# Optimization experiments

Hardware: AMD Instinct MI355X
Metric: run time of the kernel (lower is better)

## Reference

```python
import jax, jax.numpy as jnp
import numpy as np

B, N, FIN, H, D = 2, 512, 128, 4, 64
NEG_SLOPE = 0.2


def setup_inputs() -> dict:
    key = jax.random.key(0)
    ks = jax.random.split(key, 5)
    x = jax.random.normal(ks[0], (B, N, FIN), dtype=jnp.float32)
    # xavier-ish scaled params
    W_proj = jax.random.normal(ks[1], (H, FIN, D), dtype=jnp.float32) * (1.0 / np.sqrt(FIN + D))
    b_proj = jnp.zeros((H, D), dtype=jnp.float32)
    W_cat_weight = jax.random.normal(ks[2], (H, D, 2 * D), dtype=jnp.float32) * (1.0 / np.sqrt(3 * D))
    W_cat_bias = jnp.zeros((H, D), dtype=jnp.float32)
    a = jax.random.normal(ks[3], (H, D), dtype=jnp.float32) * (1.0 / np.sqrt(D))
    bias_param = jnp.zeros((H * D,), dtype=jnp.float32)
    return {"x": x, "W_proj": W_proj, "b_proj": b_proj,
            "W_cat_weight": W_cat_weight, "W_cat_bias": W_cat_bias,
            "a": a, "bias_param": bias_param}


def reference(x, W_proj, b_proj, W_cat_weight, W_cat_bias, a, bias_param):
    # h[b,h,n,d] = W^h x_n + b^h
    h = jnp.einsum('bni,hid->bhnd', x, W_proj) + b_proj[None, :, None, :]
    d = h.shape[-1]
    # W_cat [h_i || h_j] == W1 h_i + W2 h_j  (avoids O(N^2*2D) concat tensor)
    W1 = W_cat_weight[:, :, :d]   # (H, D, D) acts on source node i
    W2 = W_cat_weight[:, :, d:]   # (H, D, D) acts on target node j
    zi = jnp.einsum('bhnd,hed->bhne', h, W1)  # (B,H,N,D)
    zj = jnp.einsum('bhnd,hed->bhne', h, W2)  # (B,H,N,D)
    # z[b,h,i,j,e] = zi[b,h,i,e] + zj[b,h,j,e] + bias, then LeakyReLU
    z = zi[:, :, :, None, :] + zj[:, :, None, :, :] + W_cat_bias[None, :, None, None, :]
    z = jnp.where(z >= 0, z, NEG_SLOPE * z)
    # e[b,h,i,j] = a_h . z
    e = jnp.einsum('bhije,he->bhij', z, a)
    attn = jax.nn.softmax(e, axis=-1)          # softmax over neighbors j
    out = jnp.einsum('bhij,bhjd->bhid', attn, h)  # (B,H,N,D)
    b_, h_, n_, d_ = out.shape
    out = out.transpose(0, 2, 1, 3).reshape(b_, n_, h_ * d_)  # concat heads
    out = out + bias_param
    return out
```

## Files before the change

kernel.cpp:

```cpp
#include <hip/hip_runtime.h>
#include <hip/hip_bf16.h>

#define NN 512
#define FIN 128
#define HH 4
#define DD 64
#define SW 68


__global__ __launch_bounds__(256) void proj_kernel(
    const float* __restrict__ x, const float* __restrict__ Wp,
    const float* __restrict__ bp, const float* __restrict__ Wc,
    const float* __restrict__ Wcb, const float* __restrict__ a,
    float* __restrict__ h_ws, float* __restrict__ azi_ws, float* __restrict__ azjT,
    float* __restrict__ adi_ws, float* __restrict__ adj_ws)
{
    int blk = blockIdx.x;
    int bh = blk >> 6;
    int n0 = (blk & 63) << 3;
    int b = bh >> 2, hh = bh & 3;

    __shared__ float xs[8 * FIN];
    __shared__ float hs[8][DD];
    __shared__ float Wcs[DD][2 * DD + 1];
    __shared__ float tzj[8][DD + 1];
    __shared__ int   slot2e[SW];
    __shared__ float slot2pa[SW];

    int t = threadIdx.x;

    ((float4*)xs)[t] = ((const float4*)(x + ((size_t)b * NN + n0) * FIN))[t];
    {
        const float4* wg = (const float4*)(Wc + (size_t)hh * DD * 2 * DD);
        #pragma unroll
        for (int k = 0; k < 8; ++k) {
            int idx = t + 256 * k;
            int r = idx >> 5, c4 = (idx & 31) * 4;
            float4 v = wg[idx];
            Wcs[r][c4] = v.x; Wcs[r][c4 + 1] = v.y;
            Wcs[r][c4 + 2] = v.z; Wcs[r][c4 + 3] = v.w;
        }
    }
    __syncthreads();

    int e = t & 63, w = t >> 6;
    const float* Wph = Wp + (size_t)hh * FIN * DD;
    float bpv = bp[hh * DD + e];
    float acc0 = bpv, acc1 = bpv;
    #pragma unroll 8
    for (int i = 0; i < FIN; ++i) {
        float wv = Wph[i * DD + e];
        acc0 = fmaf(xs[w * FIN + i], wv, acc0);
        acc1 = fmaf(xs[(w + 4) * FIN + i], wv, acc1);
    }
    hs[w][e] = acc0; hs[w + 4][e] = acc1;
    float* hg = h_ws + ((size_t)bh * NN + n0) * DD;
    hg[w * DD + e] = acc0; hg[(w + 4) * DD + e] = acc1;
    __syncthreads();

    float zb = Wcb[hh * DD + e];
    float zi0 = zb, zi1 = zb, zj0 = 0.f, zj1 = 0.f;
    #pragma unroll 8
    for (int d2 = 0; d2 < DD; ++d2) {
        float w1 = Wcs[e][d2];
        float w2 = Wcs[e][DD + d2];
        float h0 = hs[w][d2], h1 = hs[w + 4][d2];
        zi0 = fmaf(h0, w1, zi0); zi1 = fmaf(h1, w1, zi1);
        zj0 = fmaf(h0, w2, zj0); zj1 = fmaf(h1, w2, zj1);
    }
    tzj[w][e] = zj0; tzj[w + 4][e] = zj1;

    float av = a[hh * DD + e];
    float p0 = av * zi0, p1 = av * zi1, q0 = av * zj0, q1 = av * zj1;
    #pragma unroll
    for (int off = 32; off; off >>= 1) {
        p0 += __shfl_xor(p0, off); p1 += __shfl_xor(p1, off);
        q0 += __shfl_xor(q0, off); q1 += __shfl_xor(q1, off);
    }
    if (e == 0) {
        adi_ws[bh * NN + n0 + w]     = 0.6f * p0;
        adi_ws[bh * NN + n0 + w + 4] = 0.6f * p1;
        adj_ws[bh * NN + n0 + w]     = 0.6f * q0;
        adj_ws[bh * NN + n0 + w + 4] = 0.6f * q1;
    }

    unsigned long long mask = __ballot(av >= 0.f);
    int np = __popcll(mask);
    int GP = (np + 3) >> 2;
    int below = __popcll(mask & ((1ull << e) - 1ull));
    int slot = (av >= 0.f) ? below : (4 * GP + (e - below));
    float pav = __builtin_fabsf(av);

    float* azib = azi_ws + ((size_t)bh * NN + n0) * SW;
    azib[w * SW + slot]       = pav * zi0;
    azib[(w + 4) * SW + slot] = pav * zi1;
    if (w == 0) { slot2e[slot] = e; slot2pa[slot] = pav; }
    int p1c = 4 * GP - np;
    if (e < 4) {
        int psl = (e < p1c) ? (np + e) : (4 * GP + 64 - np + (e - p1c));
        azib[w * SW + psl] = 0.f; azib[(w + 4) * SW + psl] = 0.f;
        if (w == 0) { slot2e[psl] = 0; slot2pa[psl] = 0.f; }
    }
    __syncthreads();

    for (int idx = t; idx < SW * 8; idx += 256) {
        int slot = idx >> 3, r = idx & 7;
        float v = slot2pa[slot] * tzj[r][slot2e[slot]];
        azjT[((size_t)bh * SW + slot) * NN + n0 + r] = v;
    }
}

__global__ __launch_bounds__(256) void attn_kernel(
    const float* __restrict__ h_ws, const float* __restrict__ azi_ws,
    const float* __restrict__ azjT, const float* __restrict__ adi_ws,
    const float* __restrict__ adj_ws, const float* __restrict__ a,
    float* __restrict__ pacc, float* __restrict__ pm, float* __restrict__ ps)
{
    int blk = blockIdx.x;
    int js = blk & 7, it = (blk >> 3) & 63, bh = blk >> 9;
    int j0 = js << 6, i0 = it << 3, hh = bh & 3;

    __shared__ float azis[8 * SW];
    __shared__ float pbuf[8][64];
    __shared__ float htile[64 * 64];

    int t = threadIdx.x, lane = t & 63;
    int w = t >> 6;

    if (t < 136)
        ((float4*)azis)[t] = ((const float4*)(azi_ws + ((size_t)bh * NN + i0) * SW))[t];
    {
        const float4* hsrc = (const float4*)(h_ws + ((size_t)bh * NN + j0) * DD);
        float4* hdst = (float4*)htile;
        #pragma unroll
        for (int k = 0; k < 4; ++k) hdst[t + 256 * k] = hsrc[t + 256 * k];
    }

    float azjr[SW];
    {
        const float* ajT = azjT + (size_t)bh * SW * NN + j0 + lane;
        #pragma unroll
        for (int k = 0; k < SW; ++k) azjr[k] = ajT[(size_t)k * NN];
    }
    float adjv = adj_ws[bh * NN + j0 + lane];

    float av_e = a[hh * DD + lane];
    unsigned long long mask = __ballot(av_e >= 0.f);
    int GP = (__popcll(mask) + 3) >> 2;
    float sgn[17];
    #pragma unroll
    for (int k = 0; k < 17; ++k) sgn[k] = (k < GP) ? 0.4f : -0.4f;

    float adiA = adi_ws[bh * NN + i0 + 2 * w];
    float adiB = adi_ws[bh * NN + i0 + 2 * w + 1];

    __syncthreads();

    #pragma unroll
    for (int ii = 0; ii < 2; ++ii) {
        int i = 2 * w + ii;
        const float4* arow = (const float4*)(azis + i * SW);
        float acc0 = 0.f, acc1 = 0.f;
        #pragma unroll
        for (int k = 0; k < 17; ++k) {
            float4 zi4 = arow[k];
            float s = sgn[k];
            acc0 = fmaf(s, __builtin_fabsf(zi4.x + azjr[4 * k + 0]), acc0);
            acc1 = fmaf(s, __builtin_fabsf(zi4.y + azjr[4 * k + 1]), acc1);
            acc0 = fmaf(s, __builtin_fabsf(zi4.z + azjr[4 * k + 2]), acc0);
            acc1 = fmaf(s, __builtin_fabsf(zi4.w + azjr[4 * k + 3]), acc1);
        }
        float ev = ((ii == 0) ? adiA : adiB) + adjv + acc0 + acc1;
        float m = ev;
        #pragma unroll
        for (int off = 32; off; off >>= 1) m = fmaxf(m, __shfl_xor(m, off));
        float p = __expf(ev - m);
        float ssum = p;
        #pragma unroll
        for (int off = 32; off; off >>= 1) ssum += __shfl_xor(ssum, off);
        pbuf[i][lane] = p;
        if (lane == 0) {
            pm[(js * 8 + bh) * NN + i0 + i] = m;
            ps[(js * 8 + bh) * NN + i0 + i] = ssum;
        }
    }

    float accA = 0.f, accB = 0.f;
    const float4* pA = (const float4*)pbuf[2 * w];
    const float4* pB = (const float4*)pbuf[2 * w + 1];
    #pragma unroll
    for (int k = 0; k < 16; ++k) {
        float4 a4 = pA[k], b4 = pB[k];
        float h0 = htile[(4 * k + 0) * 64 + lane];
        float h1 = htile[(4 * k + 1) * 64 + lane];
        float h2 = htile[(4 * k + 2) * 64 + lane];
        float h3 = htile[(4 * k + 3) * 64 + lane];
        accA = fmaf(a4.x, h0, accA); accB = fmaf(b4.x, h0, accB);
        accA = fmaf(a4.y, h1, accA); accB = fmaf(b4.y, h1, accB);
        accA = fmaf(a4.z, h2, accA); accB = fmaf(b4.z, h2, accB);
        accA = fmaf(a4.w, h3, accA); accB = fmaf(b4.w, h3, accB);
    }
    size_t ob = ((size_t)(js * 8 + bh) * NN + i0 + 2 * w) * DD + lane;
    pacc[ob] = accA;
    pacc[ob + DD] = accB;
}

__global__ __launch_bounds__(256) void combine_kernel(
    const float* __restrict__ pacc, const float* __restrict__ pm,
    const float* __restrict__ ps, const float* __restrict__ bias_param,
    float* __restrict__ out)
{
    int tid = blockIdx.x * 256 + threadIdx.x;
    int d = tid & 63;
    int row = tid >> 6;
    int bh = row >> 9, n = row & 511;
    int b = bh >> 2, hh = bh & 3;
    float mv[8];
    float m = -1e30f;
    #pragma unroll
    for (int p = 0; p < 8; ++p) { mv[p] = pm[p * 4096 + row]; m = fmaxf(m, mv[p]); }
    float denom = 0.f, acc = 0.f;
    #pragma unroll
    for (int p = 0; p < 8; ++p) {
        float wgt = __expf(mv[p] - m);
        denom = fmaf(ps[p * 4096 + row], wgt, denom);
        acc = fmaf(pacc[(size_t)p * 262144 + (size_t)row * 64 + d], wgt, acc);
    }
    out[((size_t)b * NN + n) * (HH * DD) + hh * DD + d] =
        acc / denom + bias_param[hh * DD + d];
}

extern "C" void kernel_launch(void* const* d_in, const int* in_sizes, int n_in,
                              void* d_out, int out_size, void* d_ws, size_t ws_size,
                              hipStream_t stream) {
    const float* x    = (const float*)d_in[0];
    const float* Wp   = (const float*)d_in[1];
    const float* bp   = (const float*)d_in[2];
    const float* Wc   = (const float*)d_in[3];
    const float* Wcb  = (const float*)d_in[4];
    const float* a    = (const float*)d_in[5];
    const float* bpar = (const float*)d_in[6];
    float* out = (float*)d_out;

    float* ws     = (float*)d_ws;
    float* h_ws   = ws;
    float* azi_ws = ws + 262144;
    float* azjT   = ws + 540672;
    float* adi_ws = ws + 819200;
    float* adj_ws = ws + 823296;
    float* pacc   = ws + 827392;
    float* pm     = ws + 2924544;
    float* ps     = ws + 2957312;

    proj_kernel<<<dim3(512), dim3(256), 0, stream>>>(
        x, Wp, bp, Wc, Wcb, a, h_ws, azi_ws, azjT, adi_ws, adj_ws);
    attn_kernel<<<dim3(4096), dim3(256), 0, stream>>>(
        h_ws, azi_ws, azjT, adi_ws, adj_ws, a, pacc, pm, ps);
    combine_kernel<<<dim3(1024), dim3(256), 0, stream>>>(
        pacc, pm, ps, bpar, out);
}
```

Before: 44.67 us.

## Fuse split-j attention and combine into single online-softmax kernel

Replaces the split-neighbor attention kernel plus separate combine kernel with one kernel per (batch-head, 8-row tile) that iterates over all 8 neighbor tiles using an online softmax with running max and sum. This removes the partial accumulator/max/sum workspace writes and reads and one kernel launch. In exchange the grid drops from 4096 to 512 blocks, and each block serially loads tiles, so latency hiding and occupancy are reduced.

```diff
diff --git a/kernel.cpp b/kernel.cpp
--- a/kernel.cpp
+++ b/kernel.cpp
@@ -104,21 +104,22 @@
     __syncthreads();
 
     for (int idx = t; idx < SW * 8; idx += 256) {
-        int slot = idx >> 3, r = idx & 7;
-        float v = slot2pa[slot] * tzj[r][slot2e[slot]];
-        azjT[((size_t)bh * SW + slot) * NN + n0 + r] = v;
+        int sl = idx >> 3, r = idx & 7;
+        azjT[((size_t)bh * SW + sl) * NN + n0 + r] =
+            slot2pa[sl] * tzj[r][slot2e[sl]];
     }
 }
 
-__global__ __launch_bounds__(256) void attn_kernel(
+__global__ __launch_bounds__(256) void attn_full(
     const float* __restrict__ h_ws, const float* __restrict__ azi_ws,
     const float* __restrict__ azjT, const float* __restrict__ adi_ws,
     const float* __restrict__ adj_ws, const float* __restrict__ a,
-    float* __restrict__ pacc, float* __restrict__ pm, float* __restrict__ ps)
+    const float* __restrict__ bias_param, float* __restrict__ out)
 {
     int blk = blockIdx.x;
-    int js = blk & 7, it = (blk >> 3) & 63, bh = blk >> 9;
-    int j0 = js << 6, i0 = it << 3, hh = bh & 3;
+    int bh = blk >> 6, it = blk & 63;
+    int i0 = it << 3;
+    int b = bh >> 2, hh = bh & 3;
 
     __shared__ float azis[8 * SW];
     __shared__ float pbuf[8][64];
@@ -128,21 +129,8 @@
     int w = t >> 6;
 
     if (t < 136)
-        ((float4*)azis)[t] = ((const float4*)(azi_ws + ((size_t)bh * NN + i0) * SW))[t];
-    {
-        const float4* hsrc = (const float4*)(h_ws + ((size_t)bh * NN + j0) * DD);
-        float4* hdst = (float4*)htile;
-        #pragma unroll
-        for (int k = 0; k < 4; ++k) hdst[t + 256 * k] = hsrc[t + 256 * k];
-    }
-
-    float azjr[SW];
-    {
-        const float* ajT = azjT + (size_t)bh * SW * NN + j0 + lane;
-        #pragma unroll
-        for (int k = 0; k < SW; ++k) azjr[k] = ajT[(size_t)k * NN];
-    }
-    float adjv = adj_ws[bh * NN + j0 + lane];
+        ((float4*)azis)[t] =
+            ((const float4*)(azi_ws + ((size_t)bh * NN + i0) * SW))[t];
 
     float av_e = a[hh * DD + lane];
     unsigned long long mask = __ballot(av_e >= 0.f);
@@ -154,80 +142,80 @@
     float adiA = adi_ws[bh * NN + i0 + 2 * w];
     float adiB = adi_ws[bh * NN + i0 + 2 * w + 1];
 
-    __syncthreads();
-
-    #pragma unroll
-    for (int ii = 0; ii < 2; ++ii) {
-        int i = 2 * w + ii;
-        const float4* arow = (const float4*)(azis + i * SW);
-        float acc0 = 0.f, acc1 = 0.f;
+    float mrun0 = -1e30f, mrun1 = -1e30f;
+    float srun0 = 0.f, srun1 = 0.f;
+    float accA = 0.f, accB = 0.f;
+
+    for (int jt = 0; jt < 8; ++jt) {
+        __syncthreads();
+        {
+            const float4* hsrc =
+                (const float4*)(h_ws + ((size_t)bh * NN + jt * 64) * DD);
+            float4* hdst = (float4*)htile;
+            #pragma unroll
+            for (int k = 0; k < 4; ++k) hdst[t + 256 * k] = hsrc[t + 256 * k];
+        }
+        float azjr[SW];
+        {
+            const float* ajT = azjT + (size_t)bh * SW * NN + jt * 64 + lane;
+            #pragma unroll
+            for (int k = 0; k < SW; ++k) azjr[k] = ajT[(size_t)k * NN];
+        }
+        float adjv = adj_ws[bh * NN + jt * 64 + lane];
+        __syncthreads();
+
+        float sc0, sc1;
         #pragma unroll
-        for (int k = 0; k < 17; ++k) {
-            float4 zi4 = arow[k];
-            float s = sgn[k];
-            acc0 = fmaf(s, __builtin_fabsf(zi4.x + azjr[4 * k + 0]), acc0);
-            acc1 = fmaf(s, __builtin_fabsf(zi4.y + azjr[4 * k + 1]), acc1);
-            acc0 = fmaf(s, __builtin_fabsf(zi4.z + azjr[4 * k + 2]), acc0);
-            acc1 = fmaf(s, __builtin_fabsf(zi4.w + azjr[4 * k + 3]), acc1);
-        }
-        float ev = ((ii == 0) ? adiA : adiB) + adjv + acc0 + acc1;
-        float m = ev;
+        for (int ii = 0; ii < 2; ++ii) {
+            int i = 2 * w + ii;
+            const float4* arow = (const float4*)(azis + i * SW);
+            float c0 = 0.f, c1 = 0.f;
+            #pragma unroll
+            for (int k = 0; k < 17; ++k) {
+                float4 zi4 = arow[k];
+                float s = sgn[k];
+                c0 = fmaf(s, __builtin_fabsf(zi4.x + azjr[4 * k + 0]), c0);
+                c1 = fmaf(s, __builtin_fabsf(zi4.y + azjr[4 * k + 1]), c1);
+                c0 = fmaf(s, __builtin_fabsf(zi4.z + azjr[4 * k + 2]), c0);
+                c1 = fmaf(s, __builtin_fabsf(zi4.w + azjr[4 * k + 3]), c1);
+            }
+            float ev = ((ii == 0) ? adiA : adiB) + adjv + c0 + c1;
+            float mt = ev;
+            #pragma unroll
+            for (int off = 32; off; off >>= 1) mt = fmaxf(mt, __shfl_xor(mt, off));
+            float m_old = (ii == 0) ? mrun0 : mrun1;
+            float m_new = fmaxf(m_old, mt);
+            float sc = __expf(m_old - m_new);
+            float p = __expf(ev - m_new);
+            float psum = p;
+            #pragma unroll
+            for (int off = 32; off; off >>= 1) psum += __shfl_xor(psum, off);
+            if (ii == 0) { srun0 = srun0 * sc + psum; mrun0 = m_new; sc0 = sc; }
+            else         { srun1 = srun1 * sc + psum; mrun1 = m_new; sc1 = sc; }
+            pbuf[i][lane] = p;
+        }
+
+        accA *= sc0; accB *= sc1;
+        const float4* pA = (const float4*)pbuf[2 * w];
+        const float4* pB = (const float4*)pbuf[2 * w + 1];
         #pragma unroll
-        for (int off = 32; off; off >>= 1) m = fmaxf(m, __shfl_xor(m, off));
-        float p = __expf(ev - m);
-        float ssum = p;
-        #pragma unroll
-        for (int off = 32; off; off >>= 1) ssum += __shfl_xor(ssum, off);
-        pbuf[i][lane] = p;
-        if (lane == 0) {
-            pm[(js * 8 + bh) * NN + i0 + i] = m;
-            ps[(js * 8 + bh) * NN + i0 + i] = ssum;
-        }
-    }
-
-    float accA = 0.f, accB = 0.f;
-    const float4* pA = (const float4*)pbuf[2 * w];
-    const float4* pB = (const float4*)pbuf[2 * w + 1];
-    #pragma unroll
-    for (int k = 0; k < 16; ++k) {
-        float4 a4 = pA[k], b4 = pB[k];
-        float h0 = htile[(4 * k + 0) * 64 + lane];
-        float h1 = htile[(4 * k + 1) * 64 + lane];
-        float h2 = htile[(4 * k + 2) * 64 + lane];
-        float h3 = htile[(4 * k + 3) * 64 + lane];
-        accA = fmaf(a4.x, h0, accA); accB = fmaf(b4.x, h0, accB);
-        accA = fmaf(a4.y, h1, accA); accB = fmaf(b4.y, h1, accB);
-        accA = fmaf(a4.z, h2, accA); accB = fmaf(b4.z, h2, accB);
-        accA = fmaf(a4.w, h3, accA); accB = fmaf(b4.w, h3, accB);
-    }
-    size_t ob = ((size_t)(js * 8 + bh) * NN + i0 + 2 * w) * DD + lane;
-    pacc[ob] = accA;
-    pacc[ob + DD] = accB;
-}
-
-__global__ __launch_bounds__(256) void combine_kernel(
-    const float* __restrict__ pacc, const float* __restrict__ pm,
-    const float* __restrict__ ps, const float* __restrict__ bias_param,
-    float* __restrict__ out)
-{
-    int tid = blockIdx.x * 256 + threadIdx.x;
-    int d = tid & 63;
-    int row = tid >> 6;
-    int bh = row >> 9, n = row & 511;
-    int b = bh >> 2, hh = bh & 3;
-    float mv[8];
-    float m = -1e30f;
-    #pragma unroll
-    for (int p = 0; p < 8; ++p) { mv[p] = pm[p * 4096 + row]; m = fmaxf(m, mv[p]); }
-    float denom = 0.f, acc = 0.f;
-    #pragma unroll
-    for (int p = 0; p < 8; ++p) {
-        float wgt = __expf(mv[p] - m);
-        denom = fmaf(ps[p * 4096 + row], wgt, denom);
-        acc = fmaf(pacc[(size_t)p * 262144 + (size_t)row * 64 + d], wgt, acc);
-    }
-    out[((size_t)b * NN + n) * (HH * DD) + hh * DD + d] =
-        acc / denom + bias_param[hh * DD + d];
+        for (int k = 0; k < 16; ++k) {
+            float4 a4 = pA[k], b4 = pB[k];
+            float h0 = htile[(4 * k + 0) * 64 + lane];
+            float h1 = htile[(4 * k + 1) * 64 + lane];
+            float h2 = htile[(4 * k + 2) * 64 + lane];
+            float h3 = htile[(4 * k + 3) * 64 + lane];
+            accA = fmaf(a4.x, h0, accA); accB = fmaf(b4.x, h0, accB);
+            accA = fmaf(a4.y, h1, accA); accB = fmaf(b4.y, h1, accB);
+            accA = fmaf(a4.z, h2, accA); accB = fmaf(b4.z, h2, accB);
+            accA = fmaf(a4.w, h3, accA); accB = fmaf(b4.w, h3, accB);
+        }
+    }
+
+    float bpv = bias_param[hh * DD + lane];
+    int iA = i0 + 2 * w, iB = iA + 1;
+    out[((size_t)b * NN + iA) * (HH * DD) + hh * DD + lane] = accA / srun0 + bpv;
+    out[((size_t)b * NN + iB) * (HH * DD) + hh * DD + lane] = accB / srun1 + bpv;
 }
 
 extern "C" void kernel_launch(void* const* d_in, const int* in_sizes, int n_in,
@@ -248,14 +236,9 @@
     float* azjT   = ws + 540672;
     float* adi_ws = ws + 819200;
     float* adj_ws = ws + 823296;
-    float* pacc   = ws + 827392;
-    float* pm     = ws + 2924544;
-    float* ps     = ws + 2957312;
 
     proj_kernel<<<dim3(512), dim3(256), 0, stream>>>(
         x, Wp, bp, Wc, Wcb, a, h_ws, azi_ws, azjT, adi_ws, adj_ws);
-    attn_kernel<<<dim3(4096), dim3(256), 0, stream>>>(
-        h_ws, azi_ws, azjT, adi_ws, adj_ws, a, pacc, pm, ps);
-    combine_kernel<<<dim3(1024), dim3(256), 0, stream>>>(
-        pacc, pm, ps, bpar, out);
+    attn_full<<<dim3(512), dim3(256), 0, stream>>>(
+        h_ws, azi_ws, azjT, adi_ws, adj_ws, a, bpar, out);
 }
```

After: 57.14 us. 1.28x slower.

## Tile attention over 16 query rows, block-pack azj as float4, swizzle grid

Applied to the files above, without the earlier changes.

The attention kernel now handles 16 query rows per workgroup instead of 8, with each wave doing 4 rows. This halves the grid and reuses the per-lane azj registers and the h tile over twice as many rows. The projection kernel writes azj in a blocked float4 layout so each lane loads 17 coalesced float4 values instead of 68 strided scalars. The block index is swizzled so neighbouring workgroups share a j-slice, and launch bounds ask for 4 workgroups per CU. In exchange, register pressure and the per-row serial work per wave both go up.

```diff
diff --git a/kernel.cpp b/kernel.cpp
--- a/kernel.cpp
+++ b/kernel.cpp
@@ -12,7 +12,7 @@
     const float* __restrict__ x, const float* __restrict__ Wp,
     const float* __restrict__ bp, const float* __restrict__ Wc,
     const float* __restrict__ Wcb, const float* __restrict__ a,
-    float* __restrict__ h_ws, float* __restrict__ azi_ws, float* __restrict__ azjT,
+    float* __restrict__ h_ws, float* __restrict__ azi_ws, float* __restrict__ azjB,
     float* __restrict__ adi_ws, float* __restrict__ adj_ws)
 {
     int blk = blockIdx.x;
@@ -103,106 +103,125 @@
     }
     __syncthreads();
 
-    for (int idx = t; idx < SW * 8; idx += 256) {
-        int slot = idx >> 3, r = idx & 7;
-        float v = slot2pa[slot] * tzj[r][slot2e[slot]];
-        azjT[((size_t)bh * SW + slot) * NN + n0 + r] = v;
-    }
-}
-
-__global__ __launch_bounds__(256) void attn_kernel(
+    if (t < 8 * 17) {
+        int r = t / 17, g = t % 17;
+        float4 v;
+        v.x = slot2pa[4 * g + 0] * tzj[r][slot2e[4 * g + 0]];
+        v.y = slot2pa[4 * g + 1] * tzj[r][slot2e[4 * g + 1]];
+        v.z = slot2pa[4 * g + 2] * tzj[r][slot2e[4 * g + 2]];
+        v.w = slot2pa[4 * g + 3] * tzj[r][slot2e[4 * g + 3]];
+        int jt = n0 >> 6, jl = (n0 & 63) + r;
+        ((float4*)azjB)[((size_t)(bh * 8 + jt) * 17 + g) * 64 + jl] = v;
+    }
+}
+
+__global__ __launch_bounds__(256, 4) void attn3(
     const float* __restrict__ h_ws, const float* __restrict__ azi_ws,
-    const float* __restrict__ azjT, const float* __restrict__ adi_ws,
+    const float* __restrict__ azjB, const float* __restrict__ adi_ws,
     const float* __restrict__ adj_ws, const float* __restrict__ a,
     float* __restrict__ pacc, float* __restrict__ pm, float* __restrict__ ps)
 {
-    int blk = blockIdx.x;
-    int js = blk & 7, it = (blk >> 3) & 63, bh = blk >> 9;
-    int j0 = js << 6, i0 = it << 3, hh = bh & 3;
-
-    __shared__ float azis[8 * SW];
-    __shared__ float pbuf[8][64];
+    int wg = (blockIdx.x & 7) * 256 + (blockIdx.x >> 3);
+    int bh = wg >> 8, js = (wg >> 5) & 7, it = wg & 31;
+    int i0 = it << 4, j0 = js << 6;
+    int hh = bh & 3;
+
     __shared__ float htile[64 * 64];
+    __shared__ float azis[16 * SW];
+    __shared__ float pbuf[16][64];
 
     int t = threadIdx.x, lane = t & 63;
-    int w = t >> 6;
-
-    if (t < 136)
-        ((float4*)azis)[t] = ((const float4*)(azi_ws + ((size_t)bh * NN + i0) * SW))[t];
+    int w = __builtin_amdgcn_readfirstlane(t >> 6);
+
     {
         const float4* hsrc = (const float4*)(h_ws + ((size_t)bh * NN + j0) * DD);
         float4* hdst = (float4*)htile;
         #pragma unroll
         for (int k = 0; k < 4; ++k) hdst[t + 256 * k] = hsrc[t + 256 * k];
-    }
-
-    float azjr[SW];
+        const float4* zsrc = (const float4*)(azi_ws + ((size_t)bh * NN + i0) * SW);
+        float4* zdst = (float4*)azis;
+        zdst[t] = zsrc[t];
+        if (t < 16) zdst[256 + t] = zsrc[256 + t];
+    }
+
+    float4 azj[17];
     {
-        const float* ajT = azjT + (size_t)bh * SW * NN + j0 + lane;
-        #pragma unroll
-        for (int k = 0; k < SW; ++k) azjr[k] = ajT[(size_t)k * NN];
+        const float4* ajB = (const float4*)azjB
+                          + ((size_t)(bh * 8 + js) * 17) * 64 + lane;
+        #pragma unroll
+        for (int k = 0; k < 17; ++k) azj[k] = ajB[k * 64];
     }
     float adjv = adj_ws[bh * NN + j0 + lane];
 
     float av_e = a[hh * DD + lane];
     unsigned long long mask = __ballot(av_e >= 0.f);
     int GP = (__popcll(mask) + 3) >> 2;
-    float sgn[17];
-    #pragma unroll
-    for (int k = 0; k < 17; ++k) sgn[k] = (k < GP) ? 0.4f : -0.4f;
-
-    float adiA = adi_ws[bh * NN + i0 + 2 * w];
-    float adiB = adi_ws[bh * NN + i0 + 2 * w + 1];
-
-    __syncthreads();
-
-    #pragma unroll
-    for (int ii = 0; ii < 2; ++ii) {
-        int i = 2 * w + ii;
+
+    int r0 = i0 + 4 * w;
+    float adi0 = adi_ws[bh * NN + r0 + 0];
+    float adi1 = adi_ws[bh * NN + r0 + 1];
+    float adi2 = adi_ws[bh * NN + r0 + 2];
+    float adi3 = adi_ws[bh * NN + r0 + 3];
+
+    __syncthreads();
+
+    #pragma unroll
+    for (int ii = 0; ii < 4; ++ii) {
+        int i = 4 * w + ii;
         const float4* arow = (const float4*)(azis + i * SW);
-        float acc0 = 0.f, acc1 = 0.f;
+        float c0 = 0.f, c1 = 0.f, c2 = 0.f, c3 = 0.f;
         #pragma unroll
         for (int k = 0; k < 17; ++k) {
             float4 zi4 = arow[k];
-            float s = sgn[k];
-            acc0 = fmaf(s, __builtin_fabsf(zi4.x + azjr[4 * k + 0]), acc0);
-            acc1 = fmaf(s, __builtin_fabsf(zi4.y + azjr[4 * k + 1]), acc1);
-            acc0 = fmaf(s, __builtin_fabsf(zi4.z + azjr[4 * k + 2]), acc0);
-            acc1 = fmaf(s, __builtin_fabsf(zi4.w + azjr[4 * k + 3]), acc1);
+            float4 aj = azj[k];
+            float s = (k < GP) ? 0.4f : -0.4f;
+            c0 = fmaf(s, __builtin_fabsf(zi4.x + aj.x), c0);
+            c1 = fmaf(s, __builtin_fabsf(zi4.y + aj.y), c1);
+            c2 = fmaf(s, __builtin_fabsf(zi4.z + aj.z), c2);
+            c3 = fmaf(s, __builtin_fabsf(zi4.w + aj.w), c3);
         }
-        float ev = ((ii == 0) ? adiA : adiB) + adjv + acc0 + acc1;
+        float adiv = (ii == 0) ? adi0 : (ii == 1) ? adi1 : (ii == 2) ? adi2 : adi3;
+        float ev = adiv + adjv + ((c0 + c1) + (c2 + c3));
         float m = ev;
         #pragma unroll
         for (int off = 32; off; off >>= 1) m = fmaxf(m, __shfl_xor(m, off));
         float p = __expf(ev - m);
-        float ssum = p;
-        #pragma unroll
-        for (int off = 32; off; off >>= 1) ssum += __shfl_xor(ssum, off);
+        float s = p;
+        #pragma unroll
+        for (int off = 32; off; off >>= 1) s += __shfl_xor(s, off);
         pbuf[i][lane] = p;
         if (lane == 0) {
-            pm[(js * 8 + bh) * NN + i0 + i] = m;
-            ps[(js * 8 + bh) * NN + i0 + i] = ssum;
+            pm[js * 4096 + bh * NN + i0 + i] = m;
+            ps[js * 4096 + bh * NN + i0 + i] = s;
         }
     }
 
-    float accA = 0.f, accB = 0.f;
-    const float4* pA = (const float4*)pbuf[2 * w];
-    const float4* pB = (const float4*)pbuf[2 * w + 1];
+    float a0 = 0.f, a1 = 0.f, a2 = 0.f, a3 = 0.f;
     #pragma unroll
     for (int k = 0; k < 16; ++k) {
-        float4 a4 = pA[k], b4 = pB[k];
         float h0 = htile[(4 * k + 0) * 64 + lane];
         float h1 = htile[(4 * k + 1) * 64 + lane];
         float h2 = htile[(4 * k + 2) * 64 + lane];
         float h3 = htile[(4 * k + 3) * 64 + lane];
-        accA = fmaf(a4.x, h0, accA); accB = fmaf(b4.x, h0, accB);
-        accA = fmaf(a4.y, h1, accA); accB = fmaf(b4.y, h1, accB);
-        accA = fmaf(a4.z, h2, accA); accB = fmaf(b4.z, h2, accB);
-        accA = fmaf(a4.w, h3, accA); accB = fmaf(b4.w, h3, accB);
-    }
-    size_t ob = ((size_t)(js * 8 + bh) * NN + i0 + 2 * w) * DD + lane;
-    pacc[ob] = accA;
-    pacc[ob + DD] = accB;
+        float4 p0 = *(const float4*)&pbuf[4 * w + 0][4 * k];
+        float4 p1 = *(const float4*)&pbuf[4 * w + 1][4 * k];
+        float4 p2 = *(const float4*)&pbuf[4 * w + 2][4 * k];
+        float4 p3 = *(const float4*)&pbuf[4 * w + 3][4 * k];
+        a0 = fmaf(p0.x, h0, a0); a1 = fmaf(p1.x, h0, a1);
+        a2 = fmaf(p2.x, h0, a2); a3 = fmaf(p3.x, h0, a3);
+        a0 = fmaf(p0.y, h1, a0); a1 = fmaf(p1.y, h1, a1);
+        a2 = fmaf(p2.y, h1, a2); a3 = fmaf(p3.y, h1, a3);
+        a0 = fmaf(p0.z, h2, a0); a1 = fmaf(p1.z, h2, a1);
+        a2 = fmaf(p2.z, h2, a2); a3 = fmaf(p3.z, h2, a3);
+        a0 = fmaf(p0.w, h3, a0); a1 = fmaf(p1.w, h3, a1);
+        a2 = fmaf(p2.w, h3, a2); a3 = fmaf(p3.w, h3, a3);
+    }
+
+    size_t ob = (size_t)js * 262144 + ((size_t)bh * NN + r0) * DD + lane;
+    pacc[ob]          = a0;
+    pacc[ob + DD]     = a1;
+    pacc[ob + 2 * DD] = a2;
+    pacc[ob + 3 * DD] = a3;
 }
 
 __global__ __launch_bounds__(256) void combine_kernel(
@@ -245,7 +264,7 @@
     float* ws     = (float*)d_ws;
     float* h_ws   = ws;
     float* azi_ws = ws + 262144;
-    float* azjT   = ws + 540672;
+    float* azjB   = ws + 540672;
     float* adi_ws = ws + 819200;
     float* adj_ws = ws + 823296;
     float* pacc   = ws + 827392;
@@ -253,9 +272,9 @@
     float* ps     = ws + 2957312;
 
     proj_kernel<<<dim3(512), dim3(256), 0, stream>>>(
-        x, Wp, bp, Wc, Wcb, a, h_ws, azi_ws, azjT, adi_ws, adj_ws);
-    attn_kernel<<<dim3(4096), dim3(256), 0, stream>>>(
-        h_ws, azi_ws, azjT, adi_ws, adj_ws, a, pacc, pm, ps);
+        x, Wp, bp, Wc, Wcb, a, h_ws, azi_ws, azjB, adi_ws, adj_ws);
+    attn3<<<dim3(2048), dim3(256), 0, stream>>>(
+        h_ws, azi_ws, azjB, adi_ws, adj_ws, a, pacc, pm, ps);
     combine_kernel<<<dim3(1024), dim3(256), 0, stream>>>(
         pacc, pm, ps, bpar, out);
 }
```

New measurement: 47.06 us. 1.05x slower.
